# Optimization experiments

Hardware: AMD Instinct MI355X
Metric: run time of the kernel (lower is better)

Reference implementation:

```python
import jax, jax.numpy as jnp
import numpy as np

B, L, R, E, D = 16, 28, 64, 34, 512


def setup_inputs() -> dict:
    key = jax.random.key(0)
    ks = jax.random.split(key, 10)
    logits = jax.random.uniform(ks[0], (B, L, R), dtype=jnp.float32)
    evt_embeddings = jax.random.normal(ks[1], (B, 1, D), dtype=jnp.float32)
    arg_embeddings = jax.random.normal(ks[2], (B, L, D), dtype=jnp.float32)
    # valid-arg counts in [1, L] (used as mask-count multiplier and divisor)
    arg_padding_num = jax.random.randint(ks[3], (B,), 1, L + 1).astype(jnp.float32)
    evt_type_list = jax.random.randint(ks[4], (B,), 0, E)
    s = 1.0 / np.sqrt(D)
    WRT = jax.random.normal(ks[5], (R, D, D), dtype=jnp.float32) * s
    WTT = jax.random.normal(ks[6], (E, D, D), dtype=jnp.float32) * s
    w1 = jax.random.normal(ks[7], (D, 64), dtype=jnp.float32) * s
    b1 = jnp.zeros((64,), dtype=jnp.float32)
    w2 = jax.random.normal(ks[8], (64, 1), dtype=jnp.float32) * (1.0 / 8.0)
    b2 = jnp.zeros((1,), dtype=jnp.float32)
    return {"logits": logits, "evt_embeddings": evt_embeddings,
            "arg_embeddings": arg_embeddings, "arg_padding_num": arg_padding_num,
            "evt_type_list": evt_type_list, "WRT": WRT, "WTT": WTT,
            "w1": w1, "b1": b1, "w2": w2, "b2": b2}


def reference(logits, evt_embeddings, arg_embeddings, arg_padding_num,
              evt_type_list, WRT, WTT, w1, b1, w2, b2):
    # role transition matrix per (event, arg): one-hot/soft select over WRT
    # [B,L,R] x [R,D,D] -> [B,L,D,D]  (dominant, memory-bound intermediate)
    role_mats = jnp.einsum('blr,rde->blde', logits, WRT)
    # event transition matrix: one-hot select over WTT == gather
    evt_mats = WTT[evt_type_list]                      # [B,D,D]
    # event embedding transform: [B,1,D] bmm [B,D,D] -> [B,D]
    evt_trans = jnp.einsum('bd,bde->be', evt_embeddings[:, 0, :], evt_mats)
    # per-arg transform: [B,L,D] bmm [B,L,D,D] -> [B,L,D]
    role_trans = jnp.einsum('bld,blde->ble', arg_embeddings, role_mats)
    # multiply by count, sum over args, divide by count (as in the original)
    role_trans = role_trans * arg_padding_num[:, None, None]
    new_sum = jnp.sum(role_trans, axis=1)              # [B,D]
    div = new_sum / arg_padding_num[:, None]
    graph_embeddings = (div + evt_trans) / 2.0         # [B,D]
    # scorer MLP: Linear(D,64) -> ReLU -> Linear(64,1) -> Sigmoid
    h = jax.nn.relu(graph_embeddings @ w1 + b1)
    score = jax.nn.sigmoid(h @ w2 + b2)                # [B,1]
    return score
```

## Files before the change

### kernel.cpp

```cpp
#include <hip/hip_runtime.h>
#include <math.h>

#define BB 16
#define LL 28
#define RR 64
#define DD 512
#define KK (RR * DD)
#define NCHUNK 512
#define NROLE  1024
#define NEVT   256

__global__ void __launch_bounds__(256) kernel_a(
    const float* __restrict__ logits,
    const float* __restrict__ arg,
    const float* __restrict__ WRT,
    const float* __restrict__ WTT,
    const float* __restrict__ evt_emb,
    const int*   __restrict__ evt_type,
    float* __restrict__ part,
    float* __restrict__ evt_part)
{
    __shared__ float smem[8192];
    const int t = threadIdx.x;

    if (blockIdx.x >= NROLE) {
        const int blk = blockIdx.x - NROLE;
        const int b  = blk >> 4;
        const int dc = blk & 15;
        const int d0 = dc * 32;
        const int ty = evt_type[b];
        const float* Wt = WTT + (size_t)ty * DD * DD;
        const int e4 = t & 127;
        const int s  = t >> 7;
        float4 a = {0.f, 0.f, 0.f, 0.f};
#pragma unroll
        for (int db = 0; db < 32; db += 16) {
            float  em[8];
            float4 w[8];
#pragma unroll
            for (int i = 0; i < 8; ++i) {
                const int d = d0 + db + s + 2 * i;
                em[i] = evt_emb[b * DD + d];
                w[i]  = ((const float4*)(Wt + (size_t)d * DD))[e4];
            }
#pragma unroll
            for (int i = 0; i < 8; ++i) {
                a.x = fmaf(em[i], w[i].x, a.x);
                a.y = fmaf(em[i], w[i].y, a.y);
                a.z = fmaf(em[i], w[i].z, a.z);
                a.w = fmaf(em[i], w[i].w, a.w);
            }
        }
        float4* sm4 = (float4*)smem;
        if (s == 1) sm4[e4] = a;
        __syncthreads();
        if (s == 0) {
            const float4 q = sm4[e4];
            a.x += q.x; a.y += q.y; a.z += q.z; a.w += q.w;
            ((float4*)evt_part)[(size_t)blk * 128 + e4] = a;
        }
        return;
    }

    const int blk = blockIdx.x;
    const int c  = blk >> 1;
    const int h  = blk & 1;
    const int r  = c >> 3;
    const int d0 = (c & 7) * 64;

    const int e4 = t & 63;
    const int ks = t >> 6;
    const float4* Wp = (const float4*)(WRT + ((size_t)(r * DD + d0)) * DD + h * 256);

    float4 w[8];
#pragma unroll
    for (int i = 0; i < 8; ++i)
        w[i] = Wp[(size_t)(ks + 4 * i) * 128 + e4];

    {
        const int d4 = t & 15;
        const int b  = t >> 4;
        const float4* ap = (const float4*)(arg + d0) + d4;
        float4 g = {0.f, 0.f, 0.f, 0.f};
#pragma unroll
        for (int l = 0; l < LL; ++l) {
            const float lg = logits[(b * LL + l) * RR + r];
            const float4 av = ap[(size_t)(b * LL + l) * 128];
            g.x = fmaf(lg, av.x, g.x);
            g.y = fmaf(lg, av.y, g.y);
            g.z = fmaf(lg, av.z, g.z);
            g.w = fmaf(lg, av.w, g.w);
        }
        smem[(4 * d4 + 0) * 16 + b] = g.x;
        smem[(4 * d4 + 1) * 16 + b] = g.y;
        smem[(4 * d4 + 2) * 16 + b] = g.z;
        smem[(4 * d4 + 3) * 16 + b] = g.w;
    }
    __syncthreads();

    const float4* Gl = (const float4*)smem;
    float4 acc[16];
#pragma unroll
    for (int b = 0; b < 16; ++b) acc[b] = make_float4(0.f, 0.f, 0.f, 0.f);

#pragma unroll
    for (int kb = 0; kb < 2; ++kb) {
        float4 wn[8];
        if (kb == 0) {
#pragma unroll
            for (int i = 0; i < 8; ++i)
                wn[i] = Wp[(size_t)(ks + 4 * (8 + i)) * 128 + e4];
        }
#pragma unroll
        for (int i = 0; i < 8; ++i) {
            const int kk = ks + 4 * (kb * 8 + i);
            float4 g[4];
            g[0] = Gl[kk * 4 + 0];
            g[1] = Gl[kk * 4 + 1];
            g[2] = Gl[kk * 4 + 2];
            g[3] = Gl[kk * 4 + 3];
            const float* gs = (const float*)g;
#pragma unroll
            for (int b = 0; b < 16; ++b) {
                acc[b].x = fmaf(gs[b], w[i].x, acc[b].x);
                acc[b].y = fmaf(gs[b], w[i].y, acc[b].y);
                acc[b].z = fmaf(gs[b], w[i].z, acc[b].z);
                acc[b].w = fmaf(gs[b], w[i].w, acc[b].w);
            }
        }
#pragma unroll
        for (int i = 0; i < 8; ++i) w[i] = wn[i];
    }
    __syncthreads();

    float4* sm4 = (float4*)smem;
    if (ks >= 2) {
#pragma unroll
        for (int b = 0; b < 16; ++b) sm4[(ks - 2) * 1024 + e4 * 16 + b] = acc[b];
    }
    __syncthreads();
    if (ks < 2) {
#pragma unroll
        for (int b = 0; b < 16; ++b) {
            const float4 q = sm4[ks * 1024 + e4 * 16 + b];
            acc[b].x += q.x; acc[b].y += q.y; acc[b].z += q.z; acc[b].w += q.w;
        }
    }
    __syncthreads();
    if (ks == 1) {
#pragma unroll
        for (int b = 0; b < 16; ++b) sm4[e4 * 16 + b] = acc[b];
    }
    __syncthreads();
    if (ks == 0) {
        float4* po = (float4*)part + (size_t)c * 2048;
#pragma unroll
        for (int b = 0; b < 16; ++b) {
            float4 o = acc[b];
            const float4 q = sm4[e4 * 16 + b];
            o.x += q.x; o.y += q.y; o.z += q.z; o.w += q.w;
            po[b * 128 + h * 64 + e4] = o;
        }
    }
}

__global__ void __launch_bounds__(256) kernel_reduce(
    const float* __restrict__ part,
    const float* __restrict__ evt_part,
    float* __restrict__ div_acc,
    float* __restrict__ evt_acc)
{
    const int t = threadIdx.x;
    if (blockIdx.x < 128) {
        __shared__ float4 sred[256];
        const int oo = t & 15;
        const int pg = t >> 4;
        const int o4 = blockIdx.x * 16 + oo;
        const float4* p4 = (const float4*)part;
        float4 s = {0.f, 0.f, 0.f, 0.f};
#pragma unroll 8
        for (int i = 0; i < 32; ++i) {
            const int p = pg * 32 + i;
            const float4 v = p4[(size_t)p * 2048 + o4];
            s.x += v.x; s.y += v.y; s.z += v.z; s.w += v.w;
        }
        sred[pg * 16 + oo] = s;
        __syncthreads();
        if (t < 16) {
            float4 tot = sred[t];
#pragma unroll
            for (int g = 1; g < 16; ++g) {
                const float4 v = sred[g * 16 + t];
                tot.x += v.x; tot.y += v.y; tot.z += v.z; tot.w += v.w;
            }
            ((float4*)div_acc)[blockIdx.x * 16 + t] = tot;
        }
    } else {
        const int o4 = (blockIdx.x - 128) * 256 + t;
        const int b  = o4 >> 7;
        const int el = o4 & 127;
        const float4* e4p = (const float4*)evt_part;
        float4 s = {0.f, 0.f, 0.f, 0.f};
#pragma unroll
        for (int dc = 0; dc < 16; ++dc) {
            const float4 v = e4p[(size_t)(b * 16 + dc) * 128 + el];
            s.x += v.x; s.y += v.y; s.z += v.z; s.w += v.w;
        }
        ((float4*)evt_acc)[o4] = s;
    }
}

__global__ void __launch_bounds__(256) kernel_mlp(
    const float* __restrict__ div_acc,
    const float* __restrict__ evt_acc,
    const float* __restrict__ w1,
    const float* __restrict__ b1,
    const float* __restrict__ w2,
    const float* __restrict__ b2,
    float* __restrict__ out)
{
    __shared__ float hred[256];
    const int b  = blockIdx.x;
    const int t  = threadIdx.x;
    const int j  = t & 63;
    const int dq = t >> 6;
    float hp = 0.f;
#pragma unroll 8
    for (int i = 0; i < 128; ++i) {
        const int d = dq * 128 + i;
        const float g = (div_acc[b * DD + d] + evt_acc[b * DD + d]) * 0.5f;
        hp = fmaf(g, w1[d * 64 + j], hp);
    }
    hred[t] = hp;
    __syncthreads();
    if (t < 64) {
        float h = b1[j] + hred[j] + hred[64 + j] + hred[128 + j] + hred[192 + j];
        h = fmaxf(h, 0.f);
        float v = h * w2[j];
#pragma unroll
        for (int off = 32; off > 0; off >>= 1) v += __shfl_down(v, off, 64);
        if (j == 0) out[b] = 1.f / (1.f + expf(-(v + b2[0])));
    }
}

extern "C" void kernel_launch(void* const* d_in, const int* in_sizes, int n_in,
                              void* d_out, int out_size, void* d_ws, size_t ws_size,
                              hipStream_t stream) {
    const float* logits   = (const float*)d_in[0];
    const float* evt_emb  = (const float*)d_in[1];
    const float* arg_emb  = (const float*)d_in[2];
    const int*   evt_type = (const int*)d_in[4];
    const float* WRT      = (const float*)d_in[5];
    const float* WTT      = (const float*)d_in[6];
    const float* w1       = (const float*)d_in[7];
    const float* b1       = (const float*)d_in[8];
    const float* w2       = (const float*)d_in[9];
    const float* b2       = (const float*)d_in[10];
    float* out = (float*)d_out;

    float* part     = (float*)d_ws;
    float* evt_part = part + (size_t)NCHUNK * 8192;
    float* div_acc  = evt_part + NEVT * DD;
    float* evt_acc  = div_acc + BB * DD;

    hipLaunchKernelGGL(kernel_a, dim3(NROLE + NEVT), dim3(256), 0, stream,
                       logits, arg_emb, WRT, WTT, evt_emb, evt_type, part, evt_part);
    hipLaunchKernelGGL(kernel_reduce, dim3(136), dim3(256), 0, stream,
                       part, evt_part, div_acc, evt_acc);
    hipLaunchKernelGGL(kernel_mlp, dim3(BB), dim3(256), 0, stream,
                       div_acc, evt_acc, w1, b1, w2, b2, out);
}
```

Measured before the change: 165.8 us.

## Give each role block two roles with full-width output, dropping in-block K reduction

Role blocks now each cover two roles over 64 d-rows and all 512 output columns, with threads split by batch half instead of K slice. This removes the shared-memory cross-thread reduction and cuts the number of partial chunks from 512 to 256, which shrinks the partials buffer and the reduce kernel. Event and role blocks are interleaved in the grid. The trade-off is fewer role blocks (256+256) and a longer serial K loop per block, with a runtime-indexed prefetch pointer, which may lower memory-level parallelism.

```diff
diff --git a/kernel.cpp b/kernel.cpp
--- a/kernel.cpp
+++ b/kernel.cpp
@@ -6,9 +6,8 @@
 #define RR 64
 #define DD 512
 #define KK (RR * DD)
-#define NCHUNK 512
-#define NROLE  1024
-#define NEVT   256
+#define NROLE 256
+#define NEVT  256
 
 __global__ void __launch_bounds__(256) kernel_a(
     const float* __restrict__ logits,
@@ -20,13 +19,13 @@
     float* __restrict__ part,
     float* __restrict__ evt_part)
 {
-    __shared__ float smem[8192];
-    const int t = threadIdx.x;
-
-    if (blockIdx.x >= NROLE) {
-        const int blk = blockIdx.x - NROLE;
-        const int b  = blk >> 4;
-        const int dc = blk & 15;
+    __shared__ float smem[2048];
+    const int t   = threadIdx.x;
+    const int cid = blockIdx.x >> 1;
+
+    if (blockIdx.x & 1) {
+        const int b  = cid >> 4;
+        const int dc = cid & 15;
         const int d0 = dc * 32;
         const int ty = evt_type[b];
         const float* Wt = WTT + (size_t)ty * DD * DD;
@@ -57,111 +56,97 @@
         if (s == 0) {
             const float4 q = sm4[e4];
             a.x += q.x; a.y += q.y; a.z += q.z; a.w += q.w;
-            ((float4*)evt_part)[(size_t)blk * 128 + e4] = a;
+            ((float4*)evt_part)[(size_t)cid * 128 + e4] = a;
         }
         return;
     }
 
-    const int blk = blockIdx.x;
-    const int c  = blk >> 1;
-    const int h  = blk & 1;
-    const int r  = c >> 3;
-    const int d0 = (c & 7) * 64;
-
-    const int e4 = t & 63;
-    const int ks = t >> 6;
-    const float4* Wp = (const float4*)(WRT + ((size_t)(r * DD + d0)) * DD + h * 256);
+    const int rp = cid >> 3;
+    const int r0 = rp * 2;
+    const int d0 = (cid & 7) * 64;
+
+    const float4* W0 = (const float4*)(WRT + ((size_t)r0       * DD + d0) * DD);
+    const float4* W1 = (const float4*)(WRT + ((size_t)(r0 + 1) * DD + d0) * DD);
+
+    const int e4 = t & 127;
+    const int bh = t >> 7;
 
     float4 w[8];
 #pragma unroll
     for (int i = 0; i < 8; ++i)
-        w[i] = Wp[(size_t)(ks + 4 * i) * 128 + e4];
+        w[i] = W0[(size_t)i * 128 + e4];
 
     {
+        const int b  = t >> 4;
         const int d4 = t & 15;
-        const int b  = t >> 4;
-        const float4* ap = (const float4*)(arg + d0) + d4;
-        float4 g = {0.f, 0.f, 0.f, 0.f};
-#pragma unroll
+        const float4* ap = (const float4*)(arg) + (size_t)(b * LL) * 128 + (d0 >> 2) + d4;
+        const float*  lp = logits + (b * LL) * RR + r0;
+        float4 g0 = {0.f, 0.f, 0.f, 0.f};
+        float4 g1 = {0.f, 0.f, 0.f, 0.f};
+#pragma unroll 7
         for (int l = 0; l < LL; ++l) {
-            const float lg = logits[(b * LL + l) * RR + r];
-            const float4 av = ap[(size_t)(b * LL + l) * 128];
-            g.x = fmaf(lg, av.x, g.x);
-            g.y = fmaf(lg, av.y, g.y);
-            g.z = fmaf(lg, av.z, g.z);
-            g.w = fmaf(lg, av.w, g.w);
-        }
-        smem[(4 * d4 + 0) * 16 + b] = g.x;
-        smem[(4 * d4 + 1) * 16 + b] = g.y;
-        smem[(4 * d4 + 2) * 16 + b] = g.z;
-        smem[(4 * d4 + 3) * 16 + b] = g.w;
+            const float4 av = ap[(size_t)l * 128];
+            const float l0 = lp[l * RR];
+            const float l1 = lp[l * RR + 1];
+            g0.x = fmaf(l0, av.x, g0.x); g0.y = fmaf(l0, av.y, g0.y);
+            g0.z = fmaf(l0, av.z, g0.z); g0.w = fmaf(l0, av.w, g0.w);
+            g1.x = fmaf(l1, av.x, g1.x); g1.y = fmaf(l1, av.y, g1.y);
+            g1.z = fmaf(l1, av.z, g1.z); g1.w = fmaf(l1, av.w, g1.w);
+        }
+        smem[(4 * d4 + 0) * 16 + b]        = g0.x;
+        smem[(4 * d4 + 1) * 16 + b]        = g0.y;
+        smem[(4 * d4 + 2) * 16 + b]        = g0.z;
+        smem[(4 * d4 + 3) * 16 + b]        = g0.w;
+        smem[(64 + 4 * d4 + 0) * 16 + b]   = g1.x;
+        smem[(64 + 4 * d4 + 1) * 16 + b]   = g1.y;
+        smem[(64 + 4 * d4 + 2) * 16 + b]   = g1.z;
+        smem[(64 + 4 * d4 + 3) * 16 + b]   = g1.w;
     }
     __syncthreads();
 
-    const float4* Gl = (const float4*)smem;
-    float4 acc[16];
-#pragma unroll
-    for (int b = 0; b < 16; ++b) acc[b] = make_float4(0.f, 0.f, 0.f, 0.f);
-
-#pragma unroll
-    for (int kb = 0; kb < 2; ++kb) {
+    float4 acc[8];
+#pragma unroll
+    for (int i = 0; i < 8; ++i) acc[i] = make_float4(0.f, 0.f, 0.f, 0.f);
+
+    const float* G = smem;
+    for (int kb = 0; kb < 16; ++kb) {
+        const int kbn = (kb + 1) & 15;
+        const float4* Wn = (kbn < 8) ? W0 : W1;
+        const int rbase = (kbn & 7) * 8;
         float4 wn[8];
-        if (kb == 0) {
-#pragma unroll
-            for (int i = 0; i < 8; ++i)
-                wn[i] = Wp[(size_t)(ks + 4 * (8 + i)) * 128 + e4];
-        }
+#pragma unroll
+        for (int i = 0; i < 8; ++i)
+            wn[i] = Wn[(size_t)(rbase + i) * 128 + e4];
 #pragma unroll
         for (int i = 0; i < 8; ++i) {
-            const int kk = ks + 4 * (kb * 8 + i);
-            float4 g[4];
-            g[0] = Gl[kk * 4 + 0];
-            g[1] = Gl[kk * 4 + 1];
-            g[2] = Gl[kk * 4 + 2];
-            g[3] = Gl[kk * 4 + 3];
-            const float* gs = (const float*)g;
-#pragma unroll
-            for (int b = 0; b < 16; ++b) {
-                acc[b].x = fmaf(gs[b], w[i].x, acc[b].x);
-                acc[b].y = fmaf(gs[b], w[i].y, acc[b].y);
-                acc[b].z = fmaf(gs[b], w[i].z, acc[b].z);
-                acc[b].w = fmaf(gs[b], w[i].w, acc[b].w);
-            }
+            const int kk = kb * 8 + i;
+            const float4 ga = ((const float4*)(G + kk * 16 + 8 * bh))[0];
+            const float4 gb = ((const float4*)(G + kk * 16 + 8 * bh))[1];
+            acc[0].x = fmaf(ga.x, w[i].x, acc[0].x); acc[0].y = fmaf(ga.x, w[i].y, acc[0].y);
+            acc[0].z = fmaf(ga.x, w[i].z, acc[0].z); acc[0].w = fmaf(ga.x, w[i].w, acc[0].w);
+            acc[1].x = fmaf(ga.y, w[i].x, acc[1].x); acc[1].y = fmaf(ga.y, w[i].y, acc[1].y);
+            acc[1].z = fmaf(ga.y, w[i].z, acc[1].z); acc[1].w = fmaf(ga.y, w[i].w, acc[1].w);
+            acc[2].x = fmaf(ga.z, w[i].x, acc[2].x); acc[2].y = fmaf(ga.z, w[i].y, acc[2].y);
+            acc[2].z = fmaf(ga.z, w[i].z, acc[2].z); acc[2].w = fmaf(ga.z, w[i].w, acc[2].w);
+            acc[3].x = fmaf(ga.w, w[i].x, acc[3].x); acc[3].y = fmaf(ga.w, w[i].y, acc[3].y);
+            acc[3].z = fmaf(ga.w, w[i].z, acc[3].z); acc[3].w = fmaf(ga.w, w[i].w, acc[3].w);
+            acc[4].x = fmaf(gb.x, w[i].x, acc[4].x); acc[4].y = fmaf(gb.x, w[i].y, acc[4].y);
+            acc[4].z = fmaf(gb.x, w[i].z, acc[4].z); acc[4].w = fmaf(gb.x, w[i].w, acc[4].w);
+            acc[5].x = fmaf(gb.y, w[i].x, acc[5].x); acc[5].y = fmaf(gb.y, w[i].y, acc[5].y);
+            acc[5].z = fmaf(gb.y, w[i].z, acc[5].z); acc[5].w = fmaf(gb.y, w[i].w, acc[5].w);
+            acc[6].x = fmaf(gb.z, w[i].x, acc[6].x); acc[6].y = fmaf(gb.z, w[i].y, acc[6].y);
+            acc[6].z = fmaf(gb.z, w[i].z, acc[6].z); acc[6].w = fmaf(gb.z, w[i].w, acc[6].w);
+            acc[7].x = fmaf(gb.w, w[i].x, acc[7].x); acc[7].y = fmaf(gb.w, w[i].y, acc[7].y);
+            acc[7].z = fmaf(gb.w, w[i].z, acc[7].z); acc[7].w = fmaf(gb.w, w[i].w, acc[7].w);
         }
 #pragma unroll
         for (int i = 0; i < 8; ++i) w[i] = wn[i];
     }
-    __syncthreads();
-
-    float4* sm4 = (float4*)smem;
-    if (ks >= 2) {
-#pragma unroll
-        for (int b = 0; b < 16; ++b) sm4[(ks - 2) * 1024 + e4 * 16 + b] = acc[b];
-    }
-    __syncthreads();
-    if (ks < 2) {
-#pragma unroll
-        for (int b = 0; b < 16; ++b) {
-            const float4 q = sm4[ks * 1024 + e4 * 16 + b];
-            acc[b].x += q.x; acc[b].y += q.y; acc[b].z += q.z; acc[b].w += q.w;
-        }
-    }
-    __syncthreads();
-    if (ks == 1) {
-#pragma unroll
-        for (int b = 0; b < 16; ++b) sm4[e4 * 16 + b] = acc[b];
-    }
-    __syncthreads();
-    if (ks == 0) {
-        float4* po = (float4*)part + (size_t)c * 2048;
-#pragma unroll
-        for (int b = 0; b < 16; ++b) {
-            float4 o = acc[b];
-            const float4 q = sm4[e4 * 16 + b];
-            o.x += q.x; o.y += q.y; o.z += q.z; o.w += q.w;
-            po[b * 128 + h * 64 + e4] = o;
-        }
-    }
+
+    float4* po = (float4*)part + (size_t)cid * 2048;
+#pragma unroll
+    for (int i = 0; i < 8; ++i)
+        po[(8 * bh + i) * 128 + e4] = acc[i];
 }
 
 __global__ void __launch_bounds__(256) kernel_reduce(
@@ -171,11 +156,11 @@
     float* __restrict__ evt_acc)
 {
     const int t = threadIdx.x;
-    if (blockIdx.x < 128) {
+    if (blockIdx.x < 64) {
         __shared__ float4 sred[256];
-        const int oo = t & 15;
-        const int pg = t >> 4;
-        const int o4 = blockIdx.x * 16 + oo;
+        const int oo = t & 31;
+        const int pg = t >> 5;
+        const int o4 = blockIdx.x * 32 + oo;
         const float4* p4 = (const float4*)part;
         float4 s = {0.f, 0.f, 0.f, 0.f};
 #pragma unroll 8
@@ -184,19 +169,19 @@
             const float4 v = p4[(size_t)p * 2048 + o4];
             s.x += v.x; s.y += v.y; s.z += v.z; s.w += v.w;
         }
-        sred[pg * 16 + oo] = s;
+        sred[pg * 32 + oo] = s;
         __syncthreads();
-        if (t < 16) {
+        if (t < 32) {
             float4 tot = sred[t];
 #pragma unroll
-            for (int g = 1; g < 16; ++g) {
-                const float4 v = sred[g * 16 + t];
+            for (int g = 1; g < 8; ++g) {
+                const float4 v = sred[g * 32 + t];
                 tot.x += v.x; tot.y += v.y; tot.z += v.z; tot.w += v.w;
             }
-            ((float4*)div_acc)[blockIdx.x * 16 + t] = tot;
+            ((float4*)div_acc)[blockIdx.x * 32 + t] = tot;
         }
     } else {
-        const int o4 = (blockIdx.x - 128) * 256 + t;
+        const int o4 = (blockIdx.x - 64) * 256 + t;
         const int b  = o4 >> 7;
         const int el = o4 & 127;
         const float4* e4p = (const float4*)evt_part;
@@ -259,13 +244,13 @@
     float* out = (float*)d_out;
 
     float* part     = (float*)d_ws;
-    float* evt_part = part + (size_t)NCHUNK * 8192;
+    float* evt_part = part + (size_t)NROLE * 8192;
     float* div_acc  = evt_part + NEVT * DD;
     float* evt_acc  = div_acc + BB * DD;
 
     hipLaunchKernelGGL(kernel_a, dim3(NROLE + NEVT), dim3(256), 0, stream,
                        logits, arg_emb, WRT, WTT, evt_emb, evt_type, part, evt_part);
-    hipLaunchKernelGGL(kernel_reduce, dim3(136), dim3(256), 0, stream,
+    hipLaunchKernelGGL(kernel_reduce, dim3(72), dim3(256), 0, stream,
                        part, evt_part, div_acc, evt_acc);
     hipLaunchKernelGGL(kernel_mlp, dim3(BB), dim3(256), 0, stream,
                        div_acc, evt_acc, w1, b1, w2, b2, out);
```

After: 160.6 us. 3.1% less time.
